# Kernel optimization log

Hardware: AMD Instinct MI355X
Metric: run time of the kernel (lower is better)

Reference implementation:

```python
import jax, jax.numpy as jnp
import numpy as np

N_NODES = 100000
N_EDGES = 1600000
IN_SIZE = 256
OUT_SIZE = 64


def setup_inputs() -> dict:
    key = jax.random.key(0)
    k1, k2, k3 = jax.random.split(key, 3)
    edge_index = jax.random.randint(k1, (2, N_EDGES), 0, N_NODES, dtype=jnp.int32)
    x = jax.random.normal(k2, (N_NODES, IN_SIZE), dtype=jnp.float32)
    W = jax.random.normal(k3, (OUT_SIZE, IN_SIZE), dtype=jnp.float32) * 0.05
    return {"edge_index": edge_index, "x": x, "num_nodes": N_NODES, "W": W}


def reference(edge_index, x, num_nodes, W):
    row, col = edge_index[0], edge_index[1]
    # fill_diag(adj, 1.0): drop any existing diagonal entries (value -> 0),
    # then add exactly one self-loop per node with value 1.0.
    val = jnp.where(row == col, 0.0, 1.0).astype(x.dtype)
    loops = jnp.arange(num_nodes, dtype=row.dtype)
    row_f = jnp.concatenate([row, loops])
    col_f = jnp.concatenate([col, loops])
    val_f = jnp.concatenate([val, jnp.ones((num_nodes,), dtype=x.dtype)])
    # deg = row-sum of adjacency values; D^{-1/2} with inf -> 0
    deg = jax.ops.segment_sum(val_f, row_f, num_segments=num_nodes)
    dinv = jnp.where(deg > 0, deg ** -0.5, 0.0)
    # edge weight: d^{-1/2}[row] * a * d^{-1/2}[col]
    norm = dinv[row_f] * val_f * dinv[col_f]
    # dense projection then SpMM aggregation
    xw = x @ W.T  # [N, out]
    msgs = norm[:, None] * xw[col_f]  # gather over edges [E+N, out]
    out = jax.ops.segment_sum(msgs, row_f, num_segments=num_nodes)
    return out
```

## Files before the change

kernel.cpp:

```cpp
#include <hip/hip_runtime.h>

#define IN_SIZE 256
#define OUT_SIZE 64
#define BSHIFT 7
#define BROWS 128
#define BMASK 127
#define CAP 2560
#define K1_EDGES 8192
#define WPAD 264

typedef __attribute__((ext_vector_type(8))) short short8;
typedef __attribute__((ext_vector_type(4))) float floatx4;

__device__ inline unsigned short f2bf(float f) {
  unsigned u = __builtin_bit_cast(unsigned, f);
  u += 0x7fff + ((u >> 16) & 1);
  return (unsigned short)(u >> 16);
}
__device__ inline float bf2f(unsigned short u) {
  unsigned v = (unsigned)u << 16;
  return __builtin_bit_cast(float, v);
}

__global__ __launch_bounds__(512) void zero_kernel(int* __restrict__ cursor) {
  int i = blockIdx.x * 512 + threadIdx.x;
  if (i < 1024) cursor[i] = 0;
}

struct K1SM {
  union {
    int hist[1024];
    unsigned short w[64 * WPAD];
  };
};

__global__ __launch_bounds__(512) void fused1_kernel(
    const int* __restrict__ row, const int* __restrict__ col,
    int* __restrict__ coarse_cursor, unsigned* __restrict__ pairs,
    const float* __restrict__ x, const float* __restrict__ W,
    unsigned short* __restrict__ xwb, int n_edges, int n_nodes, int nbuck,
    int nb_coarse) {
  __shared__ K1SM sm;
  int tid = threadIdx.x;
  int bid = blockIdx.x;

  if (bid < nb_coarse) {
    sm.hist[tid] = 0;
    sm.hist[tid + 512] = 0;
    __syncthreads();

    int r[16], c[16];
    int ebase = bid * K1_EDGES + tid;
#pragma unroll
    for (int i = 0; i < 16; i++) {
      int e = ebase + i * 512;
      bool ok = e < n_edges;
      r[i] = ok ? row[e] : -1;
      c[i] = ok ? col[e] : -1;
      if (ok && r[i] != c[i]) atomicAdd(&sm.hist[r[i] >> BSHIFT], 1);
    }
    __syncthreads();

    for (int i = tid; i < nbuck; i += 512) {
      int cnt = sm.hist[i];
      if (cnt) sm.hist[i] = atomicAdd(&coarse_cursor[i], cnt);
    }
    __syncthreads();

#pragma unroll
    for (int i = 0; i < 16; i++) {
      if (r[i] >= 0 && r[i] != c[i]) {
        int bin = r[i] >> BSHIFT;
        int slot = atomicAdd(&sm.hist[bin], 1);
        if (slot < CAP)
          pairs[(size_t)bin * CAP + slot] =
              ((unsigned)(r[i] & BMASK) << 17) | (unsigned)c[i];
      }
    }
  } else {
    int mb = bid - nb_coarse;
    long nbase = (long)mb * 128;
    {
      int r = tid >> 3;
      int q = tid & 7;
      const float* src = W + (size_t)r * IN_SIZE + q * 32;
#pragma unroll
      for (int i = 0; i < 4; i++) {
        float4 a = *(const float4*)(src + i * 8);
        float4 b = *(const float4*)(src + i * 8 + 4);
        short8 s;
        s[0] = (short)f2bf(a.x); s[1] = (short)f2bf(a.y);
        s[2] = (short)f2bf(a.z); s[3] = (short)f2bf(a.w);
        s[4] = (short)f2bf(b.x); s[5] = (short)f2bf(b.y);
        s[6] = (short)f2bf(b.z); s[7] = (short)f2bf(b.w);
        *(short8*)(&sm.w[r * WPAD + q * 32 + i * 8]) = s;
      }
    }
    __syncthreads();

    int wave = tid >> 6;
    int lane = tid & 63;
    int quad = lane >> 4;
    int lcol = lane & 15;
    long node = nbase + wave * 16 + lcol;
    long nclamp = (node < (long)n_nodes) ? node : (long)(n_nodes - 1);
    const float* xrow = x + nclamp * IN_SIZE;

    floatx4 acc[4];
#pragma unroll
    for (int t = 0; t < 4; t++) acc[t] = (floatx4){0.f, 0.f, 0.f, 0.f};

#pragma unroll
    for (int kk = 0; kk < 8; kk++) {
      const float* p = xrow + kk * 32 + quad * 8;
      float4 a = *(const float4*)(p);
      float4 bb = *(const float4*)(p + 4);
      short8 bfrag;
      bfrag[0] = (short)f2bf(a.x);  bfrag[1] = (short)f2bf(a.y);
      bfrag[2] = (short)f2bf(a.z);  bfrag[3] = (short)f2bf(a.w);
      bfrag[4] = (short)f2bf(bb.x); bfrag[5] = (short)f2bf(bb.y);
      bfrag[6] = (short)f2bf(bb.z); bfrag[7] = (short)f2bf(bb.w);
#pragma unroll
      for (int t = 0; t < 4; t++) {
        short8 afrag =
            *(const short8*)(&sm.w[(t * 16 + lcol) * WPAD + kk * 32 + quad * 8]);
        acc[t] = __builtin_amdgcn_mfma_f32_16x16x32_bf16(afrag, bfrag, acc[t],
                                                         0, 0, 0);
      }
    }

    if (node < (long)n_nodes) {
#pragma unroll
      for (int t = 0; t < 4; t++) {
        ushort4 sv;
        sv.x = f2bf(acc[t][0]);
        sv.y = f2bf(acc[t][1]);
        sv.z = f2bf(acc[t][2]);
        sv.w = f2bf(acc[t][3]);
        *(ushort4*)(xwb + node * OUT_SIZE + t * 16 + quad * 4) = sv;
      }
    }
  }
}

__global__ __launch_bounds__(256) void fine_kernel(
    const int* __restrict__ coarse_cursor, const unsigned* __restrict__ pairs,
    unsigned* __restrict__ colsp, int* __restrict__ count,
    int* __restrict__ row_start, float* __restrict__ dinv, int n_nodes) {
  __shared__ unsigned lpair[CAP];
  __shared__ int hist[BROWS];
  __shared__ int scn[BROWS];
  int tid = threadIdx.x;
  int b = blockIdx.x;
  size_t base = (size_t)b * CAP;
  int n_b = coarse_cursor[b];
  if (n_b > CAP) n_b = CAP;

  if (tid < BROWS) hist[tid] = 0;
  __syncthreads();

  for (int i = tid; i < n_b; i += 256) {
    unsigned p = pairs[base + i];
    lpair[i] = p;
    atomicAdd(&hist[p >> 17], 1);
  }
  __syncthreads();

  if (tid < BROWS) scn[tid] = hist[tid];
  __syncthreads();
  for (int off = 1; off < BROWS; off <<= 1) {
    int t = (tid >= off && tid < BROWS) ? scn[tid - off] : 0;
    __syncthreads();
    if (tid < BROWS) scn[tid] += t;
    __syncthreads();
  }

  if (tid < BROWS) {
    int e = (tid > 0) ? scn[tid - 1] : 0;
    int r = b * BROWS + tid;
    if (r < n_nodes) {
      int deg = hist[tid];
      count[r] = deg;
      row_start[r] = (int)base + e;
      dinv[r] = rsqrtf((float)deg + 1.0f);
    }
    hist[tid] = e;
  }
  __syncthreads();

  for (int i = tid; i < n_b; i += 256) {
    unsigned p = lpair[i];
    int slot = atomicAdd(&hist[p >> 17], 1);
    colsp[base + slot] = p & 0x1FFFFu;
  }
}

__global__ __launch_bounds__(256) void gather_kernel(
    const int* __restrict__ row_start, const int* __restrict__ count,
    const unsigned* __restrict__ colsp, const float* __restrict__ dinv,
    const unsigned short* __restrict__ xwb, float* __restrict__ out,
    int n_nodes) {
  int lane = threadIdx.x & 63;
  int wave = threadIdx.x >> 6;
  int sub = lane & 7;
  int cg = lane >> 3;
  int rb = (blockIdx.x * 4 + wave) * 4;
  if (rb >= n_nodes) return;

  int start[4], cnt[4];
  int maxc = 0;
#pragma unroll
  for (int i = 0; i < 4; i++) {
    int r = rb + i;
    bool ok = r < n_nodes;
    start[i] = ok ? row_start[r] : 0;
    cnt[i] = ok ? count[r] : 0;
    maxc = max(maxc, cnt[i]);
  }

  float acc[4][8];
#pragma unroll
  for (int i = 0; i < 4; i++)
#pragma unroll
    for (int k = 0; k < 8; k++) acc[i][k] = 0.f;

  if (sub == 0) {
#pragma unroll
    for (int i = 0; i < 4; i++) {
      int r = rb + i;
      if (r < n_nodes) {
        float dv = dinv[r];
        short8 v = *(const short8*)(xwb + (size_t)r * OUT_SIZE + cg * 8);
#pragma unroll
        for (int k = 0; k < 8; k++) acc[i][k] = dv * bf2f((unsigned short)v[k]);
      }
    }
  }

  for (int j = 0; j < maxc; j += 8) {
    int c[4];
    float m[4];
    int idx = j + sub;
#pragma unroll
    for (int i = 0; i < 4; i++) {
      bool act = idx < cnt[i];
      c[i] = act ? (int)colsp[start[i] + idx] : rb;
      m[i] = act ? dinv[c[i]] : 0.0f;
    }
    short8 v[4];
#pragma unroll
    for (int i = 0; i < 4; i++)
      v[i] = *(const short8*)(xwb + (size_t)c[i] * OUT_SIZE + cg * 8);
#pragma unroll
    for (int i = 0; i < 4; i++)
#pragma unroll
      for (int k = 0; k < 8; k++)
        acc[i][k] += m[i] * bf2f((unsigned short)v[i][k]);
  }

#pragma unroll
  for (int i = 0; i < 4; i++)
#pragma unroll
    for (int k = 0; k < 8; k++) {
      acc[i][k] += __shfl_xor(acc[i][k], 1);
      acc[i][k] += __shfl_xor(acc[i][k], 2);
      acc[i][k] += __shfl_xor(acc[i][k], 4);
    }

  if (sub == 0) {
#pragma unroll
    for (int i = 0; i < 4; i++) {
      int r = rb + i;
      if (r < n_nodes) {
        float dr = dinv[r];
        float* dst = out + (size_t)r * OUT_SIZE + cg * 8;
        *(float4*)(dst) =
            make_float4(dr * acc[i][0], dr * acc[i][1], dr * acc[i][2],
                        dr * acc[i][3]);
        *(float4*)(dst + 4) =
            make_float4(dr * acc[i][4], dr * acc[i][5], dr * acc[i][6],
                        dr * acc[i][7]);
      }
    }
  }
}

extern "C" void kernel_launch(void* const* d_in, const int* in_sizes, int n_in,
                              void* d_out, int out_size, void* d_ws,
                              size_t ws_size, hipStream_t stream) {
  const int* edge_index = (const int*)d_in[0];
  const float* x = (const float*)d_in[1];
  const float* W = (const float*)d_in[3];

  int n_edges = in_sizes[0] / 2;
  int n_nodes = in_sizes[1] / IN_SIZE;
  const int* row = edge_index;
  const int* col = edge_index + n_edges;
  float* out = (float*)d_out;

  int nbuck = (n_nodes + BROWS - 1) >> BSHIFT;
  int nb_coarse = (n_edges + K1_EDGES - 1) / K1_EDGES;
  int nb_mm = (n_nodes + 127) / 128;

  char* ws = (char*)d_ws;
  size_t nb4 = ((size_t)n_nodes * 4 + 15) & ~(size_t)15;
  int* count = (int*)ws;
  int* row_start = (int*)(ws + nb4);
  float* dinv = (float*)(ws + 2 * nb4);
  int* coarse_cursor = (int*)(ws + 3 * nb4);
  size_t pairsB = (size_t)nbuck * CAP * 4;
  unsigned* pairs = (unsigned*)(ws + 3 * nb4 + 4096);
  unsigned* colsp = (unsigned*)(ws + 3 * nb4 + 4096 + pairsB);
  unsigned short* xwb =
      (unsigned short*)(ws + 3 * nb4 + 4096 + 2 * pairsB);

  zero_kernel<<<2, 512, 0, stream>>>(coarse_cursor);
  fused1_kernel<<<nb_coarse + nb_mm, 512, 0, stream>>>(
      row, col, coarse_cursor, pairs, x, W, xwb, n_edges, n_nodes, nbuck,
      nb_coarse);
  fine_kernel<<<nbuck, 256, 0, stream>>>(coarse_cursor, pairs, colsp, count,
                                         row_start, dinv, n_nodes);
  gather_kernel<<<(n_nodes + 15) / 16, 256, 0, stream>>>(
      row_start, count, colsp, dinv, xwb, out, n_nodes);
}
```

Measured before the change: 255.8 us.

## Split matmul blocks across bucketing kernels and unroll gather loop by two

```diff
diff --git a/kernel.cpp b/kernel.cpp
--- a/kernel.cpp
+++ b/kernel.cpp
@@ -22,6 +22,74 @@
   return __builtin_bit_cast(float, v);
 }
 
+__device__ inline void matmul_body(unsigned short* w_lds,
+                                   const float* __restrict__ x,
+                                   const float* __restrict__ W,
+                                   unsigned short* __restrict__ xwb, int mb,
+                                   int n_nodes, int tid) {
+  long nbase = (long)mb * 128;
+  {
+    int r = tid >> 3;
+    int q = tid & 7;
+    const float* src = W + (size_t)r * IN_SIZE + q * 32;
+#pragma unroll
+    for (int i = 0; i < 4; i++) {
+      float4 a = *(const float4*)(src + i * 8);
+      float4 b = *(const float4*)(src + i * 8 + 4);
+      short8 s;
+      s[0] = (short)f2bf(a.x); s[1] = (short)f2bf(a.y);
+      s[2] = (short)f2bf(a.z); s[3] = (short)f2bf(a.w);
+      s[4] = (short)f2bf(b.x); s[5] = (short)f2bf(b.y);
+      s[6] = (short)f2bf(b.z); s[7] = (short)f2bf(b.w);
+      *(short8*)(&w_lds[r * WPAD + q * 32 + i * 8]) = s;
+    }
+  }
+  __syncthreads();
+
+  int wave = tid >> 6;
+  int lane = tid & 63;
+  int quad = lane >> 4;
+  int lcol = lane & 15;
+  long node = nbase + wave * 16 + lcol;
+  long nclamp = (node < (long)n_nodes) ? node : (long)(n_nodes - 1);
+  const float* xrow = x + nclamp * IN_SIZE;
+
+  floatx4 acc[4];
+#pragma unroll
+  for (int t = 0; t < 4; t++) acc[t] = (floatx4){0.f, 0.f, 0.f, 0.f};
+
+#pragma unroll
+  for (int kk = 0; kk < 8; kk++) {
+    const float* p = xrow + kk * 32 + quad * 8;
+    float4 a = *(const float4*)(p);
+    float4 bb = *(const float4*)(p + 4);
+    short8 bfrag;
+    bfrag[0] = (short)f2bf(a.x);  bfrag[1] = (short)f2bf(a.y);
+    bfrag[2] = (short)f2bf(a.z);  bfrag[3] = (short)f2bf(a.w);
+    bfrag[4] = (short)f2bf(bb.x); bfrag[5] = (short)f2bf(bb.y);
+    bfrag[6] = (short)f2bf(bb.z); bfrag[7] = (short)f2bf(bb.w);
+#pragma unroll
+    for (int t = 0; t < 4; t++) {
+      short8 afrag =
+          *(const short8*)(&w_lds[(t * 16 + lcol) * WPAD + kk * 32 + quad * 8]);
+      acc[t] = __builtin_amdgcn_mfma_f32_16x16x32_bf16(afrag, bfrag, acc[t],
+                                                       0, 0, 0);
+    }
+  }
+
+  if (node < (long)n_nodes) {
+#pragma unroll
+    for (int t = 0; t < 4; t++) {
+      ushort4 sv;
+      sv.x = f2bf(acc[t][0]);
+      sv.y = f2bf(acc[t][1]);
+      sv.z = f2bf(acc[t][2]);
+      sv.w = f2bf(acc[t][3]);
+      *(ushort4*)(xwb + node * OUT_SIZE + t * 16 + quad * 4) = sv;
+    }
+  }
+}
+
 __global__ __launch_bounds__(512) void zero_kernel(int* __restrict__ cursor) {
   int i = blockIdx.x * 512 + threadIdx.x;
   if (i < 1024) cursor[i] = 0;
@@ -34,7 +102,7 @@
   };
 };
 
-__global__ __launch_bounds__(512) void fused1_kernel(
+__global__ __launch_bounds__(512) void k1_kernel(
     const int* __restrict__ row, const int* __restrict__ col,
     int* __restrict__ coarse_cursor, unsigned* __restrict__ pairs,
     const float* __restrict__ x, const float* __restrict__ W,
@@ -78,119 +146,75 @@
       }
     }
   } else {
-    int mb = bid - nb_coarse;
-    long nbase = (long)mb * 128;
-    {
-      int r = tid >> 3;
-      int q = tid & 7;
-      const float* src = W + (size_t)r * IN_SIZE + q * 32;
-#pragma unroll
-      for (int i = 0; i < 4; i++) {
-        float4 a = *(const float4*)(src + i * 8);
-        float4 b = *(const float4*)(src + i * 8 + 4);
-        short8 s;
-        s[0] = (short)f2bf(a.x); s[1] = (short)f2bf(a.y);
-        s[2] = (short)f2bf(a.z); s[3] = (short)f2bf(a.w);
-        s[4] = (short)f2bf(b.x); s[5] = (short)f2bf(b.y);
-        s[6] = (short)f2bf(b.z); s[7] = (short)f2bf(b.w);
-        *(short8*)(&sm.w[r * WPAD + q * 32 + i * 8]) = s;
-      }
-    }
-    __syncthreads();
-
-    int wave = tid >> 6;
-    int lane = tid & 63;
-    int quad = lane >> 4;
-    int lcol = lane & 15;
-    long node = nbase + wave * 16 + lcol;
-    long nclamp = (node < (long)n_nodes) ? node : (long)(n_nodes - 1);
-    const float* xrow = x + nclamp * IN_SIZE;
-
-    floatx4 acc[4];
-#pragma unroll
-    for (int t = 0; t < 4; t++) acc[t] = (floatx4){0.f, 0.f, 0.f, 0.f};
-
-#pragma unroll
-    for (int kk = 0; kk < 8; kk++) {
-      const float* p = xrow + kk * 32 + quad * 8;
-      float4 a = *(const float4*)(p);
-      float4 bb = *(const float4*)(p + 4);
-      short8 bfrag;
-      bfrag[0] = (short)f2bf(a.x);  bfrag[1] = (short)f2bf(a.y);
-      bfrag[2] = (short)f2bf(a.z);  bfrag[3] = (short)f2bf(a.w);
-      bfrag[4] = (short)f2bf(bb.x); bfrag[5] = (short)f2bf(bb.y);
-      bfrag[6] = (short)f2bf(bb.z); bfrag[7] = (short)f2bf(bb.w);
-#pragma unroll
-      for (int t = 0; t < 4; t++) {
-        short8 afrag =
-            *(const short8*)(&sm.w[(t * 16 + lcol) * WPAD + kk * 32 + quad * 8]);
-        acc[t] = __builtin_amdgcn_mfma_f32_16x16x32_bf16(afrag, bfrag, acc[t],
-                                                         0, 0, 0);
-      }
-    }
-
-    if (node < (long)n_nodes) {
-#pragma unroll
-      for (int t = 0; t < 4; t++) {
-        ushort4 sv;
-        sv.x = f2bf(acc[t][0]);
-        sv.y = f2bf(acc[t][1]);
-        sv.z = f2bf(acc[t][2]);
-        sv.w = f2bf(acc[t][3]);
-        *(ushort4*)(xwb + node * OUT_SIZE + t * 16 + quad * 4) = sv;
-      }
-    }
-  }
-}
-
-__global__ __launch_bounds__(256) void fine_kernel(
+    matmul_body(sm.w, x, W, xwb, bid - nb_coarse, n_nodes, tid);
+  }
+}
+
+struct K2SM {
+  union {
+    struct {
+      unsigned lpair[CAP];
+      int hist[BROWS];
+      int scn[BROWS];
+    } f;
+    unsigned short w[64 * WPAD];
+  };
+};
+
+__global__ __launch_bounds__(512) void k2_kernel(
     const int* __restrict__ coarse_cursor, const unsigned* __restrict__ pairs,
     unsigned* __restrict__ colsp, int* __restrict__ count,
-    int* __restrict__ row_start, float* __restrict__ dinv, int n_nodes) {
-  __shared__ unsigned lpair[CAP];
-  __shared__ int hist[BROWS];
-  __shared__ int scn[BROWS];
+    int* __restrict__ row_start, float* __restrict__ dinv,
+    const float* __restrict__ x, const float* __restrict__ W,
+    unsigned short* __restrict__ xwb, int n_nodes, int nbuck, int mm_off) {
+  __shared__ K2SM sm;
   int tid = threadIdx.x;
   int b = blockIdx.x;
+
+  if (b >= nbuck) {
+    matmul_body(sm.w, x, W, xwb, mm_off + (b - nbuck), n_nodes, tid);
+    return;
+  }
+
   size_t base = (size_t)b * CAP;
   int n_b = coarse_cursor[b];
   if (n_b > CAP) n_b = CAP;
 
-  if (tid < BROWS) hist[tid] = 0;
-  __syncthreads();
-
-  for (int i = tid; i < n_b; i += 256) {
+  if (tid < BROWS) sm.f.hist[tid] = 0;
+  __syncthreads();
+
+  for (int i = tid; i < n_b; i += 512) {
     unsigned p = pairs[base + i];
-    lpair[i] = p;
-    atomicAdd(&hist[p >> 17], 1);
-  }
-  __syncthreads();
-
-  if (tid < BROWS) scn[tid] = hist[tid];
+    sm.f.lpair[i] = p;
+    atomicAdd(&sm.f.hist[p >> 17], 1);
+  }
+  __syncthreads();
+
+  if (tid < BROWS) sm.f.scn[tid] = sm.f.hist[tid];
   __syncthreads();
   for (int off = 1; off < BROWS; off <<= 1) {
-    int t = (tid >= off && tid < BROWS) ? scn[tid - off] : 0;
-    __syncthreads();
-    if (tid < BROWS) scn[tid] += t;
+    int t = (tid >= off && tid < BROWS) ? sm.f.scn[tid - off] : 0;
+    __syncthreads();
+    if (tid < BROWS) sm.f.scn[tid] += t;
     __syncthreads();
   }
 
   if (tid < BROWS) {
-    int e = (tid > 0) ? scn[tid - 1] : 0;
+    int e = (tid > 0) ? sm.f.scn[tid - 1] : 0;
     int r = b * BROWS + tid;
     if (r < n_nodes) {
-      int deg = hist[tid];
+      int deg = sm.f.hist[tid];
       count[r] = deg;
       row_start[r] = (int)base + e;
       dinv[r] = rsqrtf((float)deg + 1.0f);
     }
-    hist[tid] = e;
-  }
-  __syncthreads();
-
-  for (int i = tid; i < n_b; i += 256) {
-    unsigned p = lpair[i];
-    int slot = atomicAdd(&hist[p >> 17], 1);
+    sm.f.hist[tid] = e;
+  }
+  __syncthreads();
+
+  for (int i = tid; i < n_b; i += 512) {
+    unsigned p = sm.f.lpair[i];
+    int slot = atomicAdd(&sm.f.hist[p >> 17], 1);
     colsp[base + slot] = p & 0x1FFFFu;
   }
 }
@@ -237,25 +261,36 @@
     }
   }
 
-  for (int j = 0; j < maxc; j += 8) {
-    int c[4];
-    float m[4];
-    int idx = j + sub;
-#pragma unroll
-    for (int i = 0; i < 4; i++) {
-      bool act = idx < cnt[i];
-      c[i] = act ? (int)colsp[start[i] + idx] : rb;
-      m[i] = act ? dinv[c[i]] : 0.0f;
-    }
-    short8 v[4];
+  for (int j = 0; j < maxc; j += 16) {
+    int c0[4], c1[4];
+    float m0[4], m1[4];
+    int idx0 = j + sub;
+    int idx1 = idx0 + 8;
+#pragma unroll
+    for (int i = 0; i < 4; i++) {
+      bool a0 = idx0 < cnt[i];
+      bool a1 = idx1 < cnt[i];
+      c0[i] = a0 ? (int)colsp[start[i] + idx0] : rb;
+      c1[i] = a1 ? (int)colsp[start[i] + idx1] : rb;
+      m0[i] = a0 ? dinv[c0[i]] : 0.0f;
+      m1[i] = a1 ? dinv[c1[i]] : 0.0f;
+    }
+    short8 v0[4], v1[4];
+#pragma unroll
+    for (int i = 0; i < 4; i++) {
+      v0[i] = *(const short8*)(xwb + (size_t)c0[i] * OUT_SIZE + cg * 8);
+      v1[i] = *(const short8*)(xwb + (size_t)c1[i] * OUT_SIZE + cg * 8);
+    }
 #pragma unroll
     for (int i = 0; i < 4; i++)
-      v[i] = *(const short8*)(xwb + (size_t)c[i] * OUT_SIZE + cg * 8);
+#pragma unroll
+      for (int k = 0; k < 8; k++)
+        acc[i][k] += m0[i] * bf2f((unsigned short)v0[i][k]);
 #pragma unroll
     for (int i = 0; i < 4; i++)
 #pragma unroll
       for (int k = 0; k < 8; k++)
-        acc[i][k] += m[i] * bf2f((unsigned short)v[i][k]);
+        acc[i][k] += m1[i] * bf2f((unsigned short)v1[i][k]);
   }
 
 #pragma unroll
@@ -301,6 +336,7 @@
   int nbuck = (n_nodes + BROWS - 1) >> BSHIFT;
   int nb_coarse = (n_edges + K1_EDGES - 1) / K1_EDGES;
   int nb_mm = (n_nodes + 127) / 128;
+  int nmm1 = nb_mm / 2;
 
   char* ws = (char*)d_ws;
   size_t nb4 = ((size_t)n_nodes * 4 + 15) & ~(size_t)15;
@@ -315,11 +351,12 @@
       (unsigned short*)(ws + 3 * nb4 + 4096 + 2 * pairsB);
 
   zero_kernel<<<2, 512, 0, stream>>>(coarse_cursor);
-  fused1_kernel<<<nb_coarse + nb_mm, 512, 0, stream>>>(
+  k1_kernel<<<nb_coarse + nmm1, 512, 0, stream>>>(
       row, col, coarse_cursor, pairs, x, W, xwb, n_edges, n_nodes, nbuck,
       nb_coarse);
-  fine_kernel<<<nbuck, 256, 0, stream>>>(coarse_cursor, pairs, colsp, count,
-                                         row_start, dinv, n_nodes);
+  k2_kernel<<<nbuck + (nb_mm - nmm1), 512, 0, stream>>>(
+      coarse_cursor, pairs, colsp, count, row_start, dinv, x, W, xwb,
+      n_nodes, nbuck, nmm1);
   gather_kernel<<<(n_nodes + 15) / 16, 256, 0, stream>>>(
       row_start, count, colsp, dinv, xwb, out, n_nodes);
 }
```

New measurement: 267.6 us. +4.6%, slower.
